# Optimization experiments

Measured on AMD Instinct MI355X. Metric: run time of the kernel, lower is better.

## Reference

```python
import jax, jax.numpy as jnp
import numpy as np


def setup_inputs() -> dict:
    key = jax.random.key(0)
    k1, k2, k3, k4 = jax.random.split(key, 4)
    B, S, D = 32, 512, 768
    return {
        "image": jax.random.normal(k1, (B, S, D), dtype=jnp.float32),
        "text": jax.random.normal(k2, (B, S, D), dtype=jnp.float32),
        "target": jax.random.normal(k3, (B, S, D), dtype=jnp.float32),
        "padding_mask": jax.random.randint(k4, (B, S), 0, 2, dtype=jnp.int32),
    }


def reference(image, text, target, padding_mask):
    D = image.shape[-1]
    # Drop BOS / CLS position for the text<->target alignment.
    txt = text[:, 1:]                      # [B, S-1, D]
    tgt = target[:, 1:]                    # [B, S-1, D]
    pm = padding_mask[:, 1:]               # [B, S-1]

    # Cosine similarity: normalize then batched matmul.
    txt_n = txt / jnp.linalg.norm(txt, axis=-1, keepdims=True)
    tgt_n = tgt / jnp.linalg.norm(tgt, axis=-1, keepdims=True)
    sim = jnp.einsum('bid,bjd->bij', txt_n, tgt_n)   # [B, S-1, S-1]

    # For each text token, pick the best-matching target patch.
    idx = jnp.argmax(sim, axis=-1)                   # [B, S-1]
    aligned = jnp.take_along_axis(tgt, idx[..., None], axis=1)  # [B, S-1, D]

    # Masked MSE over non-padded tokens (mask==1 means padded in torch code).
    valid = (pm == 0).astype(jnp.float32)            # [B, S-1]
    diff2 = jnp.square(txt.astype(jnp.float32) - aligned.astype(jnp.float32))
    kd_text_loss = jnp.sum(diff2 * valid[..., None]) / (jnp.sum(valid) * D)

    # Plain MSE between image tokens and full target.
    kd_image_loss = jnp.mean(jnp.square(image.astype(jnp.float32) - target.astype(jnp.float32)))

    total_loss = (kd_text_loss + kd_image_loss) / 2
    return total_loss, kd_text_loss, kd_image_loss, idx
```

## Files before the change

### kernel.cpp

```cpp
#include <hip/hip_runtime.h>
#include <math.h>

#define B       32
#define S_FULL  512
#define S       511
#define D       768
#define NROWS   (B * S)

#define TM 128
#define TN 128
#define NCHUNK 4
#define NKT 24
#define RSTR 72
#define EPS_MARGIN 6e-5f

typedef __attribute__((ext_vector_type(8))) short bf16x8;
typedef __attribute__((ext_vector_type(4))) float f32x4;

__device__ inline unsigned short f2bf(float f) {
    union { float f; unsigned u; } c; c.f = f;
    unsigned u = c.u;
    return (unsigned short)((u + 0x7fffu + ((u >> 16) & 1u)) >> 16);
}
__device__ inline float bf2f(unsigned short h) {
    union { unsigned u; float f; } c; c.u = ((unsigned)h) << 16;
    return c.f;
}
__device__ inline void split4(float x0, float x1, float x2, float x3,
                              short4& hi, short4& lo) {
    unsigned short h0 = f2bf(x0), h1 = f2bf(x1), h2 = f2bf(x2), h3 = f2bf(x3);
    hi = make_short4((short)h0, (short)h1, (short)h2, (short)h3);
    lo = make_short4((short)f2bf(x0 - bf2f(h0)), (short)f2bf(x1 - bf2f(h1)),
                     (short)f2bf(x2 - bf2f(h2)), (short)f2bf(x3 - bf2f(h3)));
}

__global__ __launch_bounds__(256) void prep_kernel(
    const float* __restrict__ image, const float* __restrict__ text,
    const float* __restrict__ target,
    float* __restrict__ inv_t, float* __restrict__ inv_g, float* __restrict__ acc)
{
    int row  = blockIdx.x * 4 + (threadIdx.x >> 6);
    int lane = threadIdx.x & 63;
    int b = row >> 9, i = row & 511;
    const float4* pi4 = (const float4*)(image  + (size_t)row * D);
    const float4* pt4 = (const float4*)(text   + (size_t)row * D);
    const float4* pg4 = (const float4*)(target + (size_t)row * D);
    float st = 0.f, sg = 0.f, si = 0.f;
    #pragma unroll
    for (int q = 0; q < 3; ++q) {
        float4 a = pt4[lane + 64 * q];
        float4 g = pg4[lane + 64 * q];
        float4 m = pi4[lane + 64 * q];
        st += a.x*a.x + a.y*a.y + a.z*a.z + a.w*a.w;
        sg += g.x*g.x + g.y*g.y + g.z*g.z + g.w*g.w;
        float dx = m.x-g.x, dy = m.y-g.y, dz = m.z-g.z, dw = m.w-g.w;
        si += dx*dx + dy*dy + dz*dz + dw*dw;
    }
    #pragma unroll
    for (int m = 32; m > 0; m >>= 1) {
        st += __shfl_xor(st, m); sg += __shfl_xor(sg, m); si += __shfl_xor(si, m);
    }
    if (lane == 0) {
        atomicAdd(&acc[blockIdx.x & 63], si);
        if (i >= 1) {
            int r = b * S + i - 1;
            inv_t[r] = (st > 0.f) ? 1.f / sqrtf(st) : 0.f;
            inv_g[r] = (sg > 0.f) ? 1.f / sqrtf(sg) : 0.f;
        }
    }
}

__global__ __launch_bounds__(256, 2) void simargmax_kernel(
    const float* __restrict__ text, const float* __restrict__ target,
    const float* __restrict__ inv_t, const float* __restrict__ inv_g,
    float* __restrict__ pv, float* __restrict__ ps, int* __restrict__ pj)
{
    __shared__ __align__(16) short As[TM * RSTR];
    __shared__ __align__(16) short Bs[TM * RSTR];

    const int i0 = blockIdx.x * TM;
    const int jc = blockIdx.y;
    const int j0 = jc * TN;
    const int b  = blockIdx.z;
    const int t  = threadIdx.x;
    const int lane = t & 63;
    const int wy = t >> 6;
    const int quad = lane >> 4, cid = lane & 15;

    const float* Abase = text   + (size_t)b * S_FULL * D + D;
    const float* Bbase = target + (size_t)b * S_FULL * D + D;

    const int r0 = t >> 3;
    const int kq = (t & 7) * 4;

    float sa[4], sb[4];
    #pragma unroll
    for (int h = 0; h < 4; ++h) {
        int gi = i0 + r0 + h * 32;
        sa[h] = (gi < S) ? inv_t[b * S + gi] : 0.f;
        int gj = j0 + r0 + h * 32;
        sb[h] = (gj < S) ? inv_g[b * S + gj] : 0.f;
    }

    f32x4 acc[2][8];
    #pragma unroll
    for (int mt = 0; mt < 2; ++mt)
        #pragma unroll
        for (int nt = 0; nt < 8; ++nt)
            acc[mt][nt] = (f32x4){0.f, 0.f, 0.f, 0.f};

    for (int kt = 0; kt < NKT; ++kt) {
        const int k0 = kt * 32;
        float4 va[4], vb[4];
        #pragma unroll
        for (int h = 0; h < 4; ++h) {
            int gi = i0 + r0 + h * 32;
            va[h] = (gi < S) ? *(const float4*)(Abase + (size_t)gi * D + k0 + kq)
                             : make_float4(0.f, 0.f, 0.f, 0.f);
            int gj = j0 + r0 + h * 32;
            vb[h] = (gj < S) ? *(const float4*)(Bbase + (size_t)gj * D + k0 + kq)
                             : make_float4(0.f, 0.f, 0.f, 0.f);
        }
        __syncthreads();
        #pragma unroll
        for (int h = 0; h < 4; ++h) {
            int row = r0 + h * 32;
            short4 ahi, alo, bhi, blo;
            split4(va[h].x * sa[h], va[h].y * sa[h], va[h].z * sa[h], va[h].w * sa[h], ahi, alo);
            split4(vb[h].x * sb[h], vb[h].y * sb[h], vb[h].z * sb[h], vb[h].w * sb[h], bhi, blo);
            *(short4*)&As[row * RSTR + kq]      = ahi;
            *(short4*)&As[row * RSTR + 32 + kq] = alo;
            *(short4*)&Bs[row * RSTR + kq]      = bhi;
            *(short4*)&Bs[row * RSTR + 32 + kq] = blo;
        }
        __syncthreads();

        bf16x8 ah[2], al[2];
        #pragma unroll
        for (int mt = 0; mt < 2; ++mt) {
            int ad = (wy * 32 + mt * 16 + cid) * RSTR + quad * 8;
            ah[mt] = *(const bf16x8*)&As[ad];
            al[mt] = *(const bf16x8*)&As[ad + 32];
        }
        #pragma unroll
        for (int nt = 0; nt < 8; ++nt) {
            int bd = (nt * 16 + cid) * RSTR + quad * 8;
            bf16x8 bh = *(const bf16x8*)&Bs[bd];
            bf16x8 bl = *(const bf16x8*)&Bs[bd + 32];
            #pragma unroll
            for (int mt = 0; mt < 2; ++mt) {
                acc[mt][nt] = __builtin_amdgcn_mfma_f32_16x16x32_bf16(ah[mt], bh, acc[mt][nt], 0, 0, 0);
                acc[mt][nt] = __builtin_amdgcn_mfma_f32_16x16x32_bf16(ah[mt], bl, acc[mt][nt], 0, 0, 0);
                acc[mt][nt] = __builtin_amdgcn_mfma_f32_16x16x32_bf16(al[mt], bh, acc[mt][nt], 0, 0, 0);
            }
        }
    }

    #pragma unroll
    for (int mt = 0; mt < 2; ++mt) {
        #pragma unroll
        for (int r = 0; r < 4; ++r) {
            float v1 = -INFINITY, v2 = -INFINITY; int j1 = -1;
            #pragma unroll
            for (int nt = 0; nt < 8; ++nt) {
                int col = j0 + nt * 16 + cid;
                float v = acc[mt][nt][r];
                if (col < S) {
                    if (v > v1) { v2 = v1; v1 = v; j1 = col; }
                    else if (v > v2) v2 = v;
                }
            }
            #pragma unroll
            for (int m = 1; m < 16; m <<= 1) {
                float ov1 = __shfl_xor(v1, m);
                int   oj1 = __shfl_xor(j1, m);
                float ov2 = __shfl_xor(v2, m);
                if (ov1 > v1) { v2 = fmaxf(v1, ov2); v1 = ov1; j1 = oj1; }
                else          { v2 = fmaxf(v2, ov1); }
            }
            if (cid == 0) {
                int gi = i0 + wy * 32 + mt * 16 + quad * 4 + r;
                if (gi < S) {
                    size_t o = ((size_t)(b * S + gi) << 2) + jc;
                    pv[o] = v1; ps[o] = v2; pj[o] = j1;
                }
            }
        }
    }
}

__global__ __launch_bounds__(256) void text_kernel(
    const float* __restrict__ text, const float* __restrict__ target,
    const int* __restrict__ pm,
    const float* __restrict__ pv, const float* __restrict__ ps, const int* __restrict__ pj,
    float* __restrict__ idx_f, float* __restrict__ acc,
    int* __restrict__ list, int* __restrict__ cnt)
{
    int row = blockIdx.x * 4 + (threadIdx.x >> 6);
    if (row >= NROWS) return;
    int lane = threadIdx.x & 63;
    int b = row / S, i = row - b * S;

    float v1 = -INFINITY, v2 = -INFINITY; int j1 = 0;
    #pragma unroll
    for (int c = 0; c < NCHUNK; ++c) {
        size_t o = ((size_t)row << 2) + c;
        float a1 = pv[o], a2 = ps[o]; int aj = pj[o];
        if (a1 > v1) { v2 = fmaxf(v1, a2); v1 = a1; j1 = aj; }
        else         { v2 = fmaxf(v2, a1); }
    }
    if (v1 - v2 < EPS_MARGIN) {
        if (lane == 0) { int p = atomicAdd(cnt, 1); list[p] = row; }
        return;
    }
    if (lane == 0) idx_f[row] = (float)j1;

    if (pm[b * S_FULL + i + 1] != 0) return;
    const float4* pt = (const float4*)(text   + (size_t)(b * S_FULL + i  + 1) * D);
    const float4* pg = (const float4*)(target + (size_t)(b * S_FULL + j1 + 1) * D);
    float s = 0.f;
    #pragma unroll
    for (int q = 0; q < 3; ++q) {
        float4 a = pt[lane + 64 * q];
        float4 g = pg[lane + 64 * q];
        float dx = a.x-g.x, dy = a.y-g.y, dz = a.z-g.z, dw = a.w-g.w;
        s += dx*dx + dy*dy + dz*dz + dw*dw;
    }
    #pragma unroll
    for (int m = 32; m > 0; m >>= 1) s += __shfl_xor(s, m);
    if (lane == 0) {
        atomicAdd(&acc[64  + (blockIdx.x & 63)], s);
        atomicAdd(&acc[128 + (blockIdx.x & 63)], 1.0f);
    }
}

__global__ __launch_bounds__(256) void recheck_kernel(
    const float* __restrict__ text, const float* __restrict__ target,
    const int* __restrict__ pm, const float* __restrict__ inv_g,
    const int* __restrict__ list, const int* __restrict__ cnt,
    float* __restrict__ idx_f, float* __restrict__ acc)
{
    __shared__ float wv[4];
    __shared__ int   wj[4];
    __shared__ int   bjf;
    const int t = threadIdx.x, w = t >> 6, lane = t & 63;
    const int n = *cnt;
    for (int it = blockIdx.x; it < n; it += gridDim.x) {
        int row = list[it];
        int b = row / S, i = row - b * S;
        const float4* tp = (const float4*)(text + (size_t)(b * S_FULL + i + 1) * D);
        float4 tr0 = tp[lane], tr1 = tp[lane + 64], tr2 = tp[lane + 128];
        const float* Gb = target + (size_t)b * S_FULL * D + D;
        const float* ig = inv_g + b * S;

        float bv = -INFINITY; int bj = 0;
        for (int j = w; j < S; j += 8) {
            const float4* g0 = (const float4*)(Gb + (size_t)j * D);
            int j2 = j + 4; bool ok2 = (j2 < S);
            const float4* g1 = (const float4*)(Gb + (size_t)(ok2 ? j2 : j) * D);
            float4 a0 = g0[lane], a1 = g0[lane + 64], a2 = g0[lane + 128];
            float4 c0 = g1[lane], c1 = g1[lane + 64], c2 = g1[lane + 128];
            float s0 = tr0.x*a0.x + tr0.y*a0.y + tr0.z*a0.z + tr0.w*a0.w
                     + tr1.x*a1.x + tr1.y*a1.y + tr1.z*a1.z + tr1.w*a1.w
                     + tr2.x*a2.x + tr2.y*a2.y + tr2.z*a2.z + tr2.w*a2.w;
            float s1 = tr0.x*c0.x + tr0.y*c0.y + tr0.z*c0.z + tr0.w*c0.w
                     + tr1.x*c1.x + tr1.y*c1.y + tr1.z*c1.z + tr1.w*c1.w
                     + tr2.x*c2.x + tr2.y*c2.y + tr2.z*c2.z + tr2.w*c2.w;
            #pragma unroll
            for (int m = 32; m > 0; m >>= 1) {
                s0 += __shfl_xor(s0, m);
                s1 += __shfl_xor(s1, m);
            }
            s0 *= ig[j];
            if (s0 > bv) { bv = s0; bj = j; }
            if (ok2) {
                s1 *= ig[j2];
                if (s1 > bv) { bv = s1; bj = j2; }
            }
        }
        if (lane == 0) { wv[w] = bv; wj[w] = bj; }
        __syncthreads();
        if (t == 0) {
            float fv = wv[0]; int fj = wj[0];
            #pragma unroll
            for (int q = 1; q < 4; ++q)
                if (wv[q] > fv || (wv[q] == fv && wj[q] < fj)) { fv = wv[q]; fj = wj[q]; }
            bjf = fj;
            idx_f[row] = (float)fj;
        }
        __syncthreads();
        if (w == 0 && pm[b * S_FULL + i + 1] == 0) {
            const float4* gp = (const float4*)(Gb + (size_t)bjf * D);
            float4 a0 = gp[lane], a1 = gp[lane + 64], a2 = gp[lane + 128];
            float dx, s = 0.f;
            dx = tr0.x-a0.x; s += dx*dx;  dx = tr0.y-a0.y; s += dx*dx;
            dx = tr0.z-a0.z; s += dx*dx;  dx = tr0.w-a0.w; s += dx*dx;
            dx = tr1.x-a1.x; s += dx*dx;  dx = tr1.y-a1.y; s += dx*dx;
            dx = tr1.z-a1.z; s += dx*dx;  dx = tr1.w-a1.w; s += dx*dx;
            dx = tr2.x-a2.x; s += dx*dx;  dx = tr2.y-a2.y; s += dx*dx;
            dx = tr2.z-a2.z; s += dx*dx;  dx = tr2.w-a2.w; s += dx*dx;
            #pragma unroll
            for (int m = 32; m > 0; m >>= 1) s += __shfl_xor(s, m);
            if (lane == 0) {
                atomicAdd(&acc[64  + (blockIdx.x & 63)], s);
                atomicAdd(&acc[128 + (blockIdx.x & 63)], 1.0f);
            }
        }
        __syncthreads();
    }
}

__global__ void finalize_kernel(const float* __restrict__ acc, float* __restrict__ out)
{
    int lane = threadIdx.x;
    float si = acc[lane], st = acc[64 + lane], sc = acc[128 + lane];
    #pragma unroll
    for (int m = 32; m > 0; m >>= 1) {
        si += __shfl_xor(si, m);
        st += __shfl_xor(st, m);
        sc += __shfl_xor(sc, m);
    }
    if (lane == 0) {
        float img = si / (float)((size_t)B * S_FULL * D);
        float txt = st / (sc * (float)D);
        out[0] = 0.5f * (txt + img);
        out[1] = txt;
        out[2] = img;
    }
}

extern "C" void kernel_launch(void* const* d_in, const int* in_sizes, int n_in,
                              void* d_out, int out_size, void* d_ws, size_t ws_size,
                              hipStream_t stream) {
    const float* image  = (const float*)d_in[0];
    const float* text   = (const float*)d_in[1];
    const float* target = (const float*)d_in[2];
    const int*   pm     = (const int*)d_in[3];
    float* out = (float*)d_out;

    float* ws    = (float*)d_ws;
    float* inv_t = ws;
    float* inv_g = ws + NROWS;
    float* pv    = ws + 2 * NROWS;
    float* ps    = ws + 6 * NROWS;
    int*   pj    = (int*)(ws + 10 * NROWS);
    int*   list  = (int*)(ws + 14 * NROWS);
    int*   cnt   = (int*)(ws + 15 * NROWS);
    float* acc   = ws + 15 * NROWS + 64;

    hipMemsetAsync(ws + 15 * NROWS, 0, 256 * sizeof(float), stream);

    prep_kernel<<<B * S_FULL / 4, 256, 0, stream>>>(image, text, target, inv_t, inv_g, acc);
    simargmax_kernel<<<dim3(4, NCHUNK, B), 256, 0, stream>>>(
        text, target, inv_t, inv_g, pv, ps, pj);
    text_kernel<<<(NROWS + 3) / 4, 256, 0, stream>>>(
        text, target, pm, pv, ps, pj, out + 3, acc, list, cnt);
    recheck_kernel<<<512, 256, 0, stream>>>(
        text, target, pm, inv_g, list, cnt, out + 3, acc);
    finalize_kernel<<<1, 64, 0, stream>>>(acc, out);
}
```

Before: 357.8 us.

## Switch split-precision MFMA from bf16 to scaled fp16 with XOR-swizzled LDS

The cosine-similarity GEMM's hi/lo split moves from bf16 to fp16 MFMA, with inputs pre-scaled by 512 so they stay in fp16's normal range, and the near-tie threshold is scaled to match. The shared-memory tiles drop the padded stride of 72 for a 64-wide layout with an XOR swizzle, to avoid bank conflicts while shrinking LDS. Each thread now loads 8 contiguous floats (two float4) and converts them with native fp16 casts instead of software bf16 rounding. fp16's extra mantissa bits make the 3-MFMA split more accurate, which may send fewer rows to the tie-fallback path, at the cost of overflow/underflow risk if the scaling is off.

```diff
diff --git a/kernel.cpp b/kernel.cpp
--- a/kernel.cpp
+++ b/kernel.cpp
@@ -11,27 +11,23 @@
 #define TN 128
 #define NCHUNK 4
 #define NKT 24
-#define RSTR 72
 #define EPS_MARGIN 6e-5f
-
-typedef __attribute__((ext_vector_type(8))) short bf16x8;
+#define SIM_SCALE  512.0f
+#define SIM_SCALE2 (SIM_SCALE * SIM_SCALE)
+
+typedef __attribute__((ext_vector_type(8))) _Float16 f16x8;
 typedef __attribute__((ext_vector_type(4))) float f32x4;
 
-__device__ inline unsigned short f2bf(float f) {
-    union { float f; unsigned u; } c; c.f = f;
-    unsigned u = c.u;
-    return (unsigned short)((u + 0x7fffu + ((u >> 16) & 1u)) >> 16);
-}
-__device__ inline float bf2f(unsigned short h) {
-    union { unsigned u; float f; } c; c.u = ((unsigned)h) << 16;
-    return c.f;
-}
-__device__ inline void split4(float x0, float x1, float x2, float x3,
-                              short4& hi, short4& lo) {
-    unsigned short h0 = f2bf(x0), h1 = f2bf(x1), h2 = f2bf(x2), h3 = f2bf(x3);
-    hi = make_short4((short)h0, (short)h1, (short)h2, (short)h3);
-    lo = make_short4((short)f2bf(x0 - bf2f(h0)), (short)f2bf(x1 - bf2f(h1)),
-                     (short)f2bf(x2 - bf2f(h2)), (short)f2bf(x3 - bf2f(h3)));
+__device__ inline void cvt8(const float4& v0, const float4& v1, float s,
+                            f16x8& hv, f16x8& lv) {
+    float x[8] = {v0.x, v0.y, v0.z, v0.w, v1.x, v1.y, v1.z, v1.w};
+    #pragma unroll
+    for (int e = 0; e < 8; ++e) {
+        float xs = x[e] * s;
+        _Float16 h = (_Float16)xs;
+        hv[e] = h;
+        lv[e] = (_Float16)(xs - (float)h);
+    }
 }
 
 __global__ __launch_bounds__(256) void prep_kernel(
@@ -75,8 +71,8 @@
     const float* __restrict__ inv_t, const float* __restrict__ inv_g,
     float* __restrict__ pv, float* __restrict__ ps, int* __restrict__ pj)
 {
-    __shared__ __align__(16) short As[TM * RSTR];
-    __shared__ __align__(16) short Bs[TM * RSTR];
+    __shared__ __align__(16) _Float16 As[TM * 64];
+    __shared__ __align__(16) _Float16 Bs[TM * 64];
 
     const int i0 = blockIdx.x * TM;
     const int jc = blockIdx.y;
@@ -90,17 +86,22 @@
     const float* Abase = text   + (size_t)b * S_FULL * D + D;
     const float* Bbase = target + (size_t)b * S_FULL * D + D;
 
-    const int r0 = t >> 3;
-    const int kq = (t & 7) * 4;
-
-    float sa[4], sb[4];
-    #pragma unroll
-    for (int h = 0; h < 4; ++h) {
-        int gi = i0 + r0 + h * 32;
-        sa[h] = (gi < S) ? inv_t[b * S + gi] : 0.f;
-        int gj = j0 + r0 + h * 32;
-        sb[h] = (gj < S) ? inv_g[b * S + gj] : 0.f;
-    }
+    const int r0 = t >> 2;
+    const int c0 = t & 3;
+    const int kq = c0 * 8;
+
+    float sa[2], sb[2];
+    #pragma unroll
+    for (int h = 0; h < 2; ++h) {
+        int gi = i0 + r0 + 64 * h;
+        sa[h] = (gi < S) ? inv_t[b * S + gi] * SIM_SCALE : 0.f;
+        int gj = j0 + r0 + 64 * h;
+        sb[h] = (gj < S) ? inv_g[b * S + gj] * SIM_SCALE : 0.f;
+    }
+
+    const int sw8 = (r0 & 7) * 8;
+    const int fw8 = (cid & 7) * 8;
+    const int qh  = quad * 8;
 
     f32x4 acc[2][8];
     #pragma unroll
@@ -111,47 +112,57 @@
 
     for (int kt = 0; kt < NKT; ++kt) {
         const int k0 = kt * 32;
-        float4 va[4], vb[4];
-        #pragma unroll
-        for (int h = 0; h < 4; ++h) {
-            int gi = i0 + r0 + h * 32;
-            va[h] = (gi < S) ? *(const float4*)(Abase + (size_t)gi * D + k0 + kq)
-                             : make_float4(0.f, 0.f, 0.f, 0.f);
-            int gj = j0 + r0 + h * 32;
-            vb[h] = (gj < S) ? *(const float4*)(Bbase + (size_t)gj * D + k0 + kq)
-                             : make_float4(0.f, 0.f, 0.f, 0.f);
-        }
-        __syncthreads();
-        #pragma unroll
-        for (int h = 0; h < 4; ++h) {
-            int row = r0 + h * 32;
-            short4 ahi, alo, bhi, blo;
-            split4(va[h].x * sa[h], va[h].y * sa[h], va[h].z * sa[h], va[h].w * sa[h], ahi, alo);
-            split4(vb[h].x * sb[h], vb[h].y * sb[h], vb[h].z * sb[h], vb[h].w * sb[h], bhi, blo);
-            *(short4*)&As[row * RSTR + kq]      = ahi;
-            *(short4*)&As[row * RSTR + 32 + kq] = alo;
-            *(short4*)&Bs[row * RSTR + kq]      = bhi;
-            *(short4*)&Bs[row * RSTR + 32 + kq] = blo;
-        }
-        __syncthreads();
-
-        bf16x8 ah[2], al[2];
+        float4 va[2][2], vb[2][2];
+        #pragma unroll
+        for (int h = 0; h < 2; ++h) {
+            int gi = i0 + r0 + 64 * h;
+            if (gi < S) {
+                const float4* pa = (const float4*)(Abase + (size_t)gi * D + k0 + kq);
+                va[h][0] = pa[0]; va[h][1] = pa[1];
+            } else {
+                va[h][0] = make_float4(0.f,0.f,0.f,0.f);
+                va[h][1] = make_float4(0.f,0.f,0.f,0.f);
+            }
+            int gj = j0 + r0 + 64 * h;
+            if (gj < S) {
+                const float4* pb = (const float4*)(Bbase + (size_t)gj * D + k0 + kq);
+                vb[h][0] = pb[0]; vb[h][1] = pb[1];
+            } else {
+                vb[h][0] = make_float4(0.f,0.f,0.f,0.f);
+                vb[h][1] = make_float4(0.f,0.f,0.f,0.f);
+            }
+        }
+        __syncthreads();
+        #pragma unroll
+        for (int h = 0; h < 2; ++h) {
+            int base = (r0 + 64 * h) * 64;
+            f16x8 hv, lv;
+            cvt8(va[h][0], va[h][1], sa[h], hv, lv);
+            *(f16x8*)&As[base + (( c0 * 8      ) ^ sw8)] = hv;
+            *(f16x8*)&As[base + ((32 + c0 * 8  ) ^ sw8)] = lv;
+            cvt8(vb[h][0], vb[h][1], sb[h], hv, lv);
+            *(f16x8*)&Bs[base + (( c0 * 8      ) ^ sw8)] = hv;
+            *(f16x8*)&Bs[base + ((32 + c0 * 8  ) ^ sw8)] = lv;
+        }
+        __syncthreads();
+
+        f16x8 ah[2], al[2];
         #pragma unroll
         for (int mt = 0; mt < 2; ++mt) {
-            int ad = (wy * 32 + mt * 16 + cid) * RSTR + quad * 8;
-            ah[mt] = *(const bf16x8*)&As[ad];
-            al[mt] = *(const bf16x8*)&As[ad + 32];
+            int ad = (wy * 32 + mt * 16 + cid) * 64;
+            ah[mt] = *(const f16x8*)&As[ad + ( qh       ^ fw8)];
+            al[mt] = *(const f16x8*)&As[ad + ((32 + qh) ^ fw8)];
         }
         #pragma unroll
         for (int nt = 0; nt < 8; ++nt) {
-            int bd = (nt * 16 + cid) * RSTR + quad * 8;
-            bf16x8 bh = *(const bf16x8*)&Bs[bd];
-            bf16x8 bl = *(const bf16x8*)&Bs[bd + 32];
+            int bd = (nt * 16 + cid) * 64;
+            f16x8 bh = *(const f16x8*)&Bs[bd + ( qh       ^ fw8)];
+            f16x8 bl = *(const f16x8*)&Bs[bd + ((32 + qh) ^ fw8)];
             #pragma unroll
             for (int mt = 0; mt < 2; ++mt) {
-                acc[mt][nt] = __builtin_amdgcn_mfma_f32_16x16x32_bf16(ah[mt], bh, acc[mt][nt], 0, 0, 0);
-                acc[mt][nt] = __builtin_amdgcn_mfma_f32_16x16x32_bf16(ah[mt], bl, acc[mt][nt], 0, 0, 0);
-                acc[mt][nt] = __builtin_amdgcn_mfma_f32_16x16x32_bf16(al[mt], bh, acc[mt][nt], 0, 0, 0);
+                acc[mt][nt] = __builtin_amdgcn_mfma_f32_16x16x32_f16(ah[mt], bh, acc[mt][nt], 0, 0, 0);
+                acc[mt][nt] = __builtin_amdgcn_mfma_f32_16x16x32_f16(ah[mt], bl, acc[mt][nt], 0, 0, 0);
+                acc[mt][nt] = __builtin_amdgcn_mfma_f32_16x16x32_f16(al[mt], bh, acc[mt][nt], 0, 0, 0);
             }
         }
     }
@@ -209,7 +220,7 @@
         if (a1 > v1) { v2 = fmaxf(v1, a2); v1 = a1; j1 = aj; }
         else         { v2 = fmaxf(v2, a1); }
     }
-    if (v1 - v2 < EPS_MARGIN) {
+    if (v1 - v2 < EPS_MARGIN * SIM_SCALE2) {
         if (lane == 0) { int p = atomicAdd(cnt, 1); list[p] = row; }
         return;
     }
```

After: 348.5 us. 1.03x faster.
